# Kernel optimization log

Hardware: AMD Instinct MI355X
Metric: run time of the kernel (lower is better)

## Reference

```python
import jax, jax.numpy as jnp
import numpy as np

EMBED_DIM = 64
D_STATE = 16
D_CONV = 4
EXPAND = 2
DT_RANK = 8
D_INNER = EXPAND * EMBED_DIM  # 128
B_, T_, H_, W_ = 4, 16, 16, 16


def _causal_dwconv(x, w, b):
    # x: (B, D, L), w: (D, 1, K) depthwise causal conv (left pad K-1), matches
    # torch conv1d(padding=K-1)[..., :L]
    K = w.shape[-1]
    y = jax.lax.conv_general_dilated(
        x, w, window_strides=(1,), padding=[(K - 1, 0)],
        feature_group_count=x.shape[1], dimension_numbers=('NCH', 'OIH', 'NCH'))
    return y + b[None, :, None]


def _selective_scan(u, delta, A, Bm, Cm, D):
    # u, delta: (B, d, L); A: (d, n); Bm, Cm: (B, n, L); D: (d,)
    dA = jnp.exp(jnp.einsum('bdl,dn->lbdn', delta, A))      # (L,B,d,n)
    dBu = jnp.einsum('bdl,bnl,bdl->lbdn', delta, Bm, u)     # (L,B,d,n)
    h0 = jnp.zeros(dA.shape[1:], dA.dtype)

    def step(h, xs):
        dA_t, dBu_t = xs
        h = dA_t * h + dBu_t
        return h, h

    _, hs = jax.lax.scan(step, h0, (dA, dBu))               # (L,B,d,n)
    y = jnp.einsum('lbdn,bnl->bdl', hs, Cm)
    return y + u * D[None, :, None]


def _mamba_branch(x, z, conv_w, conv_b, xproj_w, dtproj_w, dtproj_b, A_log, D):
    # x, z: (B, d_inner, L)
    x = jax.nn.silu(_causal_dwconv(x, conv_w, conv_b))
    x_dbl = jnp.einsum('bdl,ed->bel', x, xproj_w)           # e = dt_rank + 2*n
    dt = x_dbl[:, :DT_RANK]
    Bm = x_dbl[:, DT_RANK:DT_RANK + D_STATE]
    Cm = x_dbl[:, DT_RANK + D_STATE:]
    delta = jax.nn.softplus(jnp.einsum('brl,dr->bdl', dt, dtproj_w) + dtproj_b[None, :, None])
    A = -jnp.exp(A_log)
    y = _selective_scan(x, delta, A, Bm, Cm, D)
    return y * jax.nn.silu(z)


def _conv3d(x, w, b, pad):
    y = jax.lax.conv_general_dilated(
        x, w, window_strides=(1, 1, 1), padding=[(pad, pad)] * 3,
        dimension_numbers=('NCDHW', 'OIDHW', 'NCDHW'))
    return y + b[None, :, None, None, None]


def setup_inputs() -> dict:
    key = jax.random.key(0)
    ks = jax.random.split(key, 24)
    s = 0.02
    d, n, r, K, C = D_INNER, D_STATE, DT_RANK, D_CONV, EMBED_DIM
    inp = {
        'x': jax.random.normal(ks[0], (B_, C, T_, H_, W_), jnp.float32),
        'in_proj_w': jax.random.normal(ks[1], (2 * d, C), jnp.float32) * s,
        'conv_w': jax.random.normal(ks[2], (d, 1, K), jnp.float32) * s,
        'conv_b': jnp.zeros((d,), jnp.float32),
        'xproj_w': jax.random.normal(ks[3], (r + 2 * n, d), jnp.float32) * s,
        'dtproj_w': jax.random.normal(ks[4], (d, r), jnp.float32) * s,
        'dtproj_b': jax.random.normal(ks[5], (d,), jnp.float32) * s,
        'A_log': jnp.tile(jnp.log(jnp.arange(1, n + 1, dtype=jnp.float32))[None, :], (d, 1)),
        'D': jnp.ones((d,), jnp.float32),
        'conv_w_b': jax.random.normal(ks[6], (d, 1, K), jnp.float32) * s,
        'conv_b_b': jnp.zeros((d,), jnp.float32),
        'xproj_w_b': jax.random.normal(ks[7], (r + 2 * n, d), jnp.float32) * s,
        'dtproj_w_b': jax.random.normal(ks[8], (d, r), jnp.float32) * s,
        'dtproj_b_b': jax.random.normal(ks[9], (d,), jnp.float32) * s,
        'A_b_log': jnp.tile(jnp.log(jnp.arange(1, n + 1, dtype=jnp.float32))[None, :], (d, 1)),
        'D_b': jnp.ones((d,), jnp.float32),
        'out_proj_w': jax.random.normal(ks[10], (C, d), jnp.float32) * s,
        'proj_w': jax.random.normal(ks[11], (C, C, 3, 3, 3), jnp.float32) * s,
        'proj_b': jnp.zeros((C,), jnp.float32),
        'norm_w': jax.random.normal(ks[12], (C, C, 1, 1, 1), jnp.float32) * s,
        'norm_b': jnp.zeros((C,), jnp.float32),
    }
    return inp


def reference(x, in_proj_w, conv_w, conv_b, xproj_w, dtproj_w, dtproj_b, A_log, D,
              conv_w_b, conv_b_b, xproj_w_b, dtproj_w_b, dtproj_b_b, A_b_log, D_b,
              out_proj_w, proj_w, proj_b, norm_w, norm_b):
    residual = x
    B, C, T, H, W = x.shape
    # SpectralPriority scan: b c t h w -> b c (h w t)
    seq = x.transpose(0, 1, 3, 4, 2).reshape(B, C, H * W * T)
    # bimamba v2
    xz = jnp.einsum('bcl,ec->bel', seq, in_proj_w)          # (B, 2*d_inner, L)
    x_f, z_f = xz[:, :D_INNER], xz[:, D_INNER:]
    y_f = _mamba_branch(x_f, z_f, conv_w, conv_b, xproj_w, dtproj_w, dtproj_b, A_log, D)
    xz_r = jnp.flip(xz, -1)
    x_b, z_b = xz_r[:, :D_INNER], xz_r[:, D_INNER:]
    y_b = _mamba_branch(x_b, z_b, conv_w_b, conv_b_b, xproj_w_b, dtproj_w_b, dtproj_b_b, A_b_log, D_b)
    out = y_f + jnp.flip(y_b, -1)                           # (B, d_inner, L)
    out = jnp.einsum('bdl,cd->blc', out, out_proj_w)        # (B, L, C)
    x_recon = out.reshape(B, C, T, H, W)
    x3 = _conv3d(x_recon, proj_w, proj_b, pad=1)
    return _conv3d(x3 + residual, norm_w, norm_b, pad=0)
```

## Files before the change

### kernel.cpp

```cpp
#include <hip/hip_runtime.h>


#define NL 4096

typedef unsigned short u16;
typedef unsigned int u32;
typedef __attribute__((ext_vector_type(8))) short bf16x8;
typedef __attribute__((ext_vector_type(4))) float f32x4;

__device__ __forceinline__ float siluf_(float x) {
  return x * __builtin_amdgcn_rcpf(1.f + __expf(-x));
}
__device__ __forceinline__ float softplusf_(float x) {
  return (x > 20.f) ? x : __logf(1.f + __expf(x));
}
__device__ __forceinline__ u16 f2bf(float f) {
  u32 u = __float_as_uint(f);
  u += 0x7fffu + ((u >> 16) & 1u);
  return (u16)(u >> 16);
}
__device__ __forceinline__ float bflo(u32 v) { return __uint_as_float(v << 16); }
__device__ __forceinline__ float bfhi(u32 v) { return __uint_as_float(v & 0xFFFF0000u); }

__device__ __forceinline__ float rowsum16_(float p) {
  int q;
  q = __builtin_amdgcn_mov_dpp(__float_as_int(p), 0x121, 0xf, 0xf, false);
  p += __int_as_float(q);
  q = __builtin_amdgcn_mov_dpp(__float_as_int(p), 0x122, 0xf, 0xf, false);
  p += __int_as_float(q);
  q = __builtin_amdgcn_mov_dpp(__float_as_int(p), 0x124, 0xf, 0xf, false);
  p += __int_as_float(q);
  q = __builtin_amdgcn_mov_dpp(__float_as_int(p), 0x128, 0xf, 0xf, false);
  p += __int_as_float(q);
  return p;
}

#define OXZ  0u
#define OUCF 1048576u
#define OUCB 1572864u
#define ODLF 2424832u
#define ODLB 2949120u
#define OYF  3473408u
#define OYB  3997696u
#define OO   4521984u
#define OO2  5046272u
#define OX4  5308416u
#define PER_B 5570560u

#define NCH 64
#define CL  64

__global__ __launch_bounds__(256) void kxz(
    const float* __restrict__ x, const float* __restrict__ wip,
    float* __restrict__ ws, int b0) {
  int bi = blockIdx.y, gb = b0 + bi;
  float* s = ws + (size_t)bi * PER_B;
  int bid = blockIdx.x;
  int h = bid >> 4, w = bid & 15;
  int tid = threadIdx.x;
  __shared__ float xs[64][16];
  for (int i = tid; i < 1024; i += 256) {
    int c = i >> 4, t = i & 15;
    xs[c][t] = x[(size_t)(gb * 64 + c) * NL + t * 256 + h * 16 + w];
  }
  __syncthreads();
  int e = tid;
  float acc[16];
#pragma unroll
  for (int t = 0; t < 16; ++t) acc[t] = 0.f;
  for (int c = 0; c < 64; ++c) {
    float wv = wip[e * 64 + c];
#pragma unroll
    for (int t = 0; t < 16; ++t) acc[t] = fmaf(wv, xs[c][t], acc[t]);
  }
  float4* dst = (float4*)(s + OXZ + (size_t)e * NL + h * 256 + w * 16);
#pragma unroll
  for (int q = 0; q < 4; ++q)
    dst[q] = make_float4(acc[q * 4], acc[q * 4 + 1], acc[q * 4 + 2], acc[q * 4 + 3]);
}

__global__ __launch_bounds__(256) void k2prep(
    const float* __restrict__ cwf, const float* __restrict__ cbf,
    const float* __restrict__ xpf, const float* __restrict__ dtwf,
    const float* __restrict__ dtbf,
    const float* __restrict__ cwb, const float* __restrict__ cbb,
    const float* __restrict__ xpb, const float* __restrict__ dtwb,
    const float* __restrict__ dtbb,
    float* __restrict__ ws) {
  int bi = blockIdx.y;
  float* s = ws + (size_t)bi * PER_B;
  int bx = blockIdx.x;
  int lt = bx >> 1, dir = bx & 1;
  int l0 = lt * 32;
  int lout0 = dir ? (127 - lt) * 32 : l0;
  int tid = threadIdx.x;

  __shared__ float pool[128 * 40];
  __shared__ u16 uct[32][136];
  float (*X)[40] = (float(*)[40])pool;

  for (int i = tid; i < 128 * 38; i += 256) {
    int d = i / 38, j = i - d * 38;
    int l = l0 - 3 + j;
    X[d][j] = (l >= 0 && l < NL) ? s[OXZ + (size_t)d * NL + l] : 0.f;
  }
  __syncthreads();

  const float* cw = dir ? cwb : cwf;
  const float* cb = dir ? cbb : cbf;
  u16* ucg = (u16*)(s + (dir ? OUCB : OUCF));
  for (int i = tid; i < 128 * 32; i += 256) {
    int d = i >> 5, li = i & 31;
    float a = cb[d];
    if (dir == 0) {
#pragma unroll
      for (int k = 0; k < 4; ++k) a = fmaf(cw[d * 4 + k], X[d][li + k], a);
    } else {
#pragma unroll
      for (int k = 0; k < 4; ++k) a = fmaf(cw[d * 4 + k], X[d][37 - li - k], a);
    }
    a = siluf_(a);
    u16 ab = f2bf(a);
    uct[li][d] = ab;
    ucg[(size_t)d * NL + lout0 + li] = ab;
  }
  __syncthreads();

  float* xds = pool;
  {
    int wid = tid >> 6, lane = tid & 63;
    int n16 = lane & 15, kg = lane >> 4;
    const float* xp = dir ? xpb : xpf;
#pragma unroll
    for (int rep = 0; rep < 2; ++rep) {
      int id = wid + rep * 4;
      if (id < 6) {
        int et = id >> 1, lt2 = id & 1;
        f32x4 acc = {};
#pragma unroll
        for (int ks = 0; ks < 4; ++ks) {
          bf16x8 bfrag = *(const bf16x8*)&uct[lt2 * 16 + n16][ks * 32 + kg * 8];
          int e = et * 16 + n16;
          int ec = (e < 40) ? e : 39;
          const float* pa = xp + ec * 128 + ks * 32 + kg * 8;
          float4 a0 = *(const float4*)pa;
          float4 a1 = *(const float4*)(pa + 4);
          bf16x8 af;
          af[0] = (short)f2bf(a0.x); af[1] = (short)f2bf(a0.y);
          af[2] = (short)f2bf(a0.z); af[3] = (short)f2bf(a0.w);
          af[4] = (short)f2bf(a1.x); af[5] = (short)f2bf(a1.y);
          af[6] = (short)f2bf(a1.z); af[7] = (short)f2bf(a1.w);
          acc = __builtin_amdgcn_mfma_f32_16x16x32_bf16(af, bfrag, acc, 0, 0, 0);
        }
#pragma unroll
        for (int rg = 0; rg < 4; ++rg) {
          int e = et * 16 + kg * 4 + rg;
          if (e < 40) xds[e * 33 + lt2 * 16 + n16] = acc[rg];
        }
      }
    }
  }
  __syncthreads();

  const float* dtw = dir ? dtwb : dtwf;
  const float* dtb = dir ? dtbb : dtbf;
  u16* dlg = (u16*)(s + (dir ? ODLB : ODLF));
  for (int i = tid; i < 128 * 32; i += 256) {
    int d = i >> 5, li = i & 31;
    float pre = dtb[d];
#pragma unroll
    for (int r = 0; r < 8; ++r)
      pre = fmaf(dtw[d * 8 + r], xds[r * 33 + li], pre);
    dlg[(size_t)d * NL + lout0 + li] = f2bf(softplusf_(pre));
  }
  u16* bctp = (u16*)(s + OO2);
  for (int i = tid; i < 32 * 32; i += 256) {
    int li = i >> 5, k = i & 31;
    bctp[((size_t)dir * 4096 + lout0 + li) * 32 + k] = f2bf(xds[(8 + k) * 33 + li]);
  }
}

__global__ __launch_bounds__(256) void kscanA(
    const float* __restrict__ Alf, const float* __restrict__ Alb,
    float* __restrict__ ws) {
  int bi = blockIdx.y;
  float* s = ws + (size_t)bi * PER_B;
  int xid = blockIdx.x;
  int chunk = xid >> 4, dir = (xid >> 3) & 1, d8 = xid & 7;
  int tid = threadIdx.x;
  int wv = tid >> 6, lane = tid & 63;
  int n = lane & 15, g = lane >> 4;
  int d = d8 * 16 + wv * 4 + g;
  int l0 = chunk * CL;
  __shared__ float bl[CL * 32];
  {
    const u16* bctp = (const u16*)(s + OO2) + ((size_t)dir * 4096 + l0) * 32;
    for (int i = tid; i < CL * 32; i += 256)
      bl[i] = __uint_as_float(((u32)bctp[i]) << 16);
  }
  __syncthreads();
  const u16* ucp = (const u16*)(s + (dir ? OUCB : OUCF)) + (size_t)d * NL + l0;
  const u16* dlp = (const u16*)(s + (dir ? ODLB : ODLF)) + (size_t)d * NL + l0;
  float A = -__expf((dir ? Alb : Alf)[d * 16 + n]);
  float P = 1.f, S = 0.f;
  for (int i0 = 0; i0 < CL; i0 += 8) {
    uint4 dq = *(const uint4*)(dlp + i0);
    uint4 uq = *(const uint4*)(ucp + i0);
    float dv[8] = {bflo(dq.x), bfhi(dq.x), bflo(dq.y), bfhi(dq.y),
                   bflo(dq.z), bfhi(dq.z), bflo(dq.w), bfhi(dq.w)};
    float uv[8] = {bflo(uq.x), bfhi(uq.x), bflo(uq.y), bfhi(uq.y),
                   bflo(uq.z), bfhi(uq.z), bflo(uq.w), bfhi(uq.w)};
#pragma unroll
    for (int j = 0; j < 8; ++j) {
      float dA = __expf(dv[j] * A);
      S = fmaf(dA, S, dv[j] * bl[(i0 + j) * 32 + n] * uv[j]);
      P *= dA;
    }
  }
  size_t cidx = ((size_t)(chunk * 2 + dir) * 128 + d) * 16 + n;
  s[OO + cidx] = P;
  s[OO + 262144u + cidx] = S;
}

__global__ __launch_bounds__(64) void kscanB(float* __restrict__ ws) {
  int bi = blockIdx.y;
  float* s = ws + (size_t)bi * PER_B;
  int dir = blockIdx.x >> 5, dblk = blockIdx.x & 31;
  int tid = threadIdx.x;
  size_t base = (size_t)dir * 2048 + dblk * 64 + tid;
  float carry = 0.f;
#pragma unroll 4
  for (int c = 0; c < NCH; ++c) {
    size_t idx = (size_t)c * 4096 + base;
    float pv = s[OO + idx], sv = s[OO + 262144u + idx];
    s[OO + 262144u + idx] = carry;
    carry = fmaf(pv, carry, sv);
  }
}

__global__ __launch_bounds__(256) void kscanC(
    const float* __restrict__ Alf, const float* __restrict__ Df,
    const float* __restrict__ Alb, const float* __restrict__ Db,
    float* __restrict__ ws) {
  int bi = blockIdx.y;
  float* s = ws + (size_t)bi * PER_B;
  int xid = blockIdx.x;
  int chunk = xid >> 4, dir = (xid >> 3) & 1, d8 = xid & 7;
  int tid = threadIdx.x;
  int wv = tid >> 6, lane = tid & 63;
  int n = lane & 15, g = lane >> 4;
  int d = d8 * 16 + wv * 4 + g;
  int l0 = chunk * CL;
  __shared__ float bl[CL * 32];
  __shared__ float ps[16][65];
  {
    const u16* bctp = (const u16*)(s + OO2) + ((size_t)dir * 4096 + l0) * 32;
    for (int i = tid; i < CL * 32; i += 256)
      bl[i] = __uint_as_float(((u32)bctp[i]) << 16);
  }
  __syncthreads();
  const u16* ucp = (const u16*)(s + (dir ? OUCB : OUCF)) + (size_t)d * NL + l0;
  const u16* dlp = (const u16*)(s + (dir ? ODLB : ODLF)) + (size_t)d * NL + l0;
  float* ybase = s + (dir ? OYB : OYF);
  float A = -__expf((dir ? Alb : Alf)[d * 16 + n]);
  float Dv = (dir ? Db : Df)[d];
  size_t cidx = ((size_t)(chunk * 2 + dir) * 128 + d) * 16 + n;
  float h = s[OO + 262144u + cidx];
  int prow = wv * 4 + g;
  for (int i0 = 0; i0 < CL; i0 += 8) {
    uint4 dq = *(const uint4*)(dlp + i0);
    uint4 uq = *(const uint4*)(ucp + i0);
    float dv[8] = {bflo(dq.x), bfhi(dq.x), bflo(dq.y), bfhi(dq.y),
                   bflo(dq.z), bfhi(dq.z), bflo(dq.w), bfhi(dq.w)};
    float uv[8] = {bflo(uq.x), bfhi(uq.x), bflo(uq.y), bfhi(uq.y),
                   bflo(uq.z), bfhi(uq.z), bflo(uq.w), bfhi(uq.w)};
#pragma unroll
    for (int j = 0; j < 8; ++j) {
      int i = i0 + j;
      float dA = __expf(dv[j] * A);
      h = fmaf(dA, h, dv[j] * bl[i * 32 + n] * uv[j]);
      float p = rowsum16_(h * bl[i * 32 + 16 + n]);
      if (n == 0) ps[prow][i] = fmaf(uv[j], Dv, p);
    }
  }
  __syncthreads();
  for (int i = tid; i < 16 * CL; i += 256) {
    int row = i >> 6, col = i & 63;
    ybase[(size_t)(d8 * 16 + row) * NL + l0 + col] = ps[row][col];
  }
}

__global__ __launch_bounds__(256) void koutg(
    const float* __restrict__ wout, float* __restrict__ ws) {
  int bi = blockIdx.y;
  float* s = ws + (size_t)bi * PER_B;
  int lt = blockIdx.x;
  int l0 = lt * 32;
  int tid = threadIdx.x;
  __shared__ float ot[128][32];
  __shared__ float ot2[64][33];
  for (int i = tid; i < 128 * 32; i += 256) {
    int d = i >> 5, li = i & 31;
    int l = l0 + li;
    float z = s[OXZ + (size_t)(128 + d) * NL + l];
    float v = s[OYF + (size_t)d * NL + l] + s[OYB + (size_t)d * NL + (NL - 1 - l)];
    ot[d][li] = v * siluf_(z);
  }
  __syncthreads();
  {
    int li = tid & 31, cg = tid >> 5;
    float acc[8];
#pragma unroll
    for (int j = 0; j < 8; ++j) acc[j] = 0.f;
    for (int d4 = 0; d4 < 128; d4 += 4) {
      float o0 = ot[d4][li], o1 = ot[d4 + 1][li];
      float o2v = ot[d4 + 2][li], o3 = ot[d4 + 3][li];
#pragma unroll
      for (int j = 0; j < 8; ++j) {
        float4 w4 = *(const float4*)&wout[(cg * 8 + j) * 128 + d4];
        acc[j] = fmaf(w4.x, o0, fmaf(w4.y, o1, fmaf(w4.z, o2v, fmaf(w4.w, o3, acc[j]))));
      }
    }
#pragma unroll
    for (int j = 0; j < 8; ++j) ot2[cg * 8 + j][li] = acc[j];
  }
  __syncthreads();
  for (int i = tid; i < 32 * 64; i += 256) {
    int li = i >> 6, c = i & 63;
    s[OO2 + (size_t)(l0 + li) * 64 + c] = ot2[c][li];
  }
}

__global__ __launch_bounds__(256) void kprepw(
    const float* __restrict__ pw, float* __restrict__ ws) {
  int off = blockIdx.x;
  u16* wb = (u16*)(ws + OO);
  int tid = threadIdx.x;
  for (int i = tid; i < 4096; i += 256) {
    int co = i >> 6, ci = i & 63;
    wb[off * 4096 + i] = f2bf(pw[(size_t)(co * 64 + ci) * 27 + off]);
  }
}

__global__ __launch_bounds__(256) void kconv3(
    const float* __restrict__ pb, const float* __restrict__ xin,
    float* __restrict__ ws, int b0) {
  int bi = blockIdx.y, gb = b0 + bi;
  float* s = ws + (size_t)bi * PER_B;
  int t = blockIdx.x >> 2, hq = blockIdx.x & 3;
  int h0 = hq * 4;
  int tid = threadIdx.x;
  const u16* wb = (const u16*)(ws + OO);
  const float* xr = s + OO2;

  __shared__ u16 Xs[3 * 6 * 18 * 72];
  {
    u32* xz32 = (u32*)Xs;
    for (int i = tid; i < 3 * 6 * 18 * 72 / 2; i += 256) xz32[i] = 0u;
  }
  __syncthreads();
  {
    int ci = tid >> 2, wq = tid & 3;
    for (int row = 0; row < 18; ++row) {
      int tt = row / 6, hh = row - tt * 6;
      int ts = t + tt - 1, hs = h0 + hh - 1;
      if (ts < 0 || ts > 15 || hs < 0 || hs > 15) continue;
      float4 v = *(const float4*)(xr + (size_t)ci * NL + ts * 256 + hs * 16 + wq * 4);
      int rb = (tt * 6 + hh) * 18 + 1 + wq * 4;
      Xs[(rb + 0) * 72 + ci] = f2bf(v.x);
      Xs[(rb + 1) * 72 + ci] = f2bf(v.y);
      Xs[(rb + 2) * 72 + ci] = f2bf(v.z);
      Xs[(rb + 3) * 72 + ci] = f2bf(v.w);
    }
  }
  __syncthreads();

  int wid = tid >> 6, lane = tid & 63;
  int cb = wid >> 1, lb = wid & 1;
  int n16 = lane & 15, kg = lane >> 4;
  f32x4 acc[2][2] = {};

  const u16* wbA = wb + (size_t)(cb * 32 + n16) * 64 + kg * 8;
  for (int kt = 0; kt < 3; ++kt)
    for (int kh = 0; kh < 3; ++kh) {
      int rbase = (kt * 6 + lb * 2 + kh) * 18 + n16;
#pragma unroll
      for (int kw = 0; kw < 3; ++kw) {
        int off = (kt * 3 + kh) * 3 + kw;
        int r0 = rbase + kw;
        const u16* pa = wbA + off * 4096;
#pragma unroll
        for (int st = 0; st < 2; ++st) {
          int kb = st * 32;
          bf16x8 a0 = *(const bf16x8*)(pa + kb);
          bf16x8 a1 = *(const bf16x8*)(pa + 16 * 64 + kb);
          bf16x8 b0 = *(const bf16x8*)(&Xs[r0 * 72 + kb + kg * 8]);
          bf16x8 b1 = *(const bf16x8*)(&Xs[(r0 + 18) * 72 + kb + kg * 8]);
          acc[0][0] = __builtin_amdgcn_mfma_f32_16x16x32_bf16(a0, b0, acc[0][0], 0, 0, 0);
          acc[0][1] = __builtin_amdgcn_mfma_f32_16x16x32_bf16(a0, b1, acc[0][1], 0, 0, 0);
          acc[1][0] = __builtin_amdgcn_mfma_f32_16x16x32_bf16(a1, b0, acc[1][0], 0, 0, 0);
          acc[1][1] = __builtin_amdgcn_mfma_f32_16x16x32_bf16(a1, b1, acc[1][1], 0, 0, 0);
        }
      }
    }

#pragma unroll
  for (int c2 = 0; c2 < 2; ++c2) {
#pragma unroll
    for (int l2 = 0; l2 < 2; ++l2) {
      int lg = t * 256 + (h0 + lb * 2 + l2) * 16 + n16;
#pragma unroll
      for (int rg = 0; rg < 4; ++rg) {
        int co = cb * 32 + c2 * 16 + kg * 4 + rg;
        float v = acc[c2][l2][rg] + pb[co] +
                  xin[(size_t)(gb * 64 + co) * NL + lg];
        s[OX4 + (size_t)co * NL + lg] = v;
      }
    }
  }
}

__global__ __launch_bounds__(256) void knorm(
    const float* __restrict__ nw, const float* __restrict__ nb,
    float* __restrict__ out, float* __restrict__ ws, int b0) {
  int bi = blockIdx.y, gb = b0 + bi;
  float* s = ws + (size_t)bi * PER_B;
  int pt = blockIdx.x;
  int p0 = pt * 64;
  int tid = threadIdx.x;
  __shared__ float xs[64][64];
  for (int i = tid; i < 4096; i += 256) {
    int ci = i >> 6, p = i & 63;
    xs[ci][p] = s[OX4 + (size_t)ci * NL + p0 + p];
  }
  __syncthreads();
  int co = tid >> 2, pq = tid & 3;
  float acc[16];
#pragma unroll
  for (int j = 0; j < 16; ++j) acc[j] = 0.f;
  for (int ci = 0; ci < 64; ci += 4) {
    float4 w4 = *(const float4*)&nw[co * 64 + ci];
    float wv[4] = {w4.x, w4.y, w4.z, w4.w};
#pragma unroll
    for (int cc = 0; cc < 4; ++cc) {
      const float4* row = (const float4*)&xs[ci + cc][pq * 16];
      float4 a = row[0], b = row[1], c = row[2], e = row[3];
      acc[0] = fmaf(wv[cc], a.x, acc[0]);  acc[1] = fmaf(wv[cc], a.y, acc[1]);
      acc[2] = fmaf(wv[cc], a.z, acc[2]);  acc[3] = fmaf(wv[cc], a.w, acc[3]);
      acc[4] = fmaf(wv[cc], b.x, acc[4]);  acc[5] = fmaf(wv[cc], b.y, acc[5]);
      acc[6] = fmaf(wv[cc], b.z, acc[6]);  acc[7] = fmaf(wv[cc], b.w, acc[7]);
      acc[8] = fmaf(wv[cc], c.x, acc[8]);  acc[9] = fmaf(wv[cc], c.y, acc[9]);
      acc[10] = fmaf(wv[cc], c.z, acc[10]); acc[11] = fmaf(wv[cc], c.w, acc[11]);
      acc[12] = fmaf(wv[cc], e.x, acc[12]); acc[13] = fmaf(wv[cc], e.y, acc[13]);
      acc[14] = fmaf(wv[cc], e.z, acc[14]); acc[15] = fmaf(wv[cc], e.w, acc[15]);
    }
  }
  float bias = nb[co];
  float4* dst = (float4*)(out + (size_t)(gb * 64 + co) * NL + p0 + pq * 16);
#pragma unroll
  for (int q = 0; q < 4; ++q)
    dst[q] = make_float4(acc[q * 4] + bias, acc[q * 4 + 1] + bias,
                         acc[q * 4 + 2] + bias, acc[q * 4 + 3] + bias);
}

extern "C" void kernel_launch(void* const* d_in, const int* in_sizes, int n_in,
                              void* d_out, int out_size, void* d_ws, size_t ws_size,
                              hipStream_t stream) {
  const float* x    = (const float*)d_in[0];
  const float* wip  = (const float*)d_in[1];
  const float* cwf  = (const float*)d_in[2];
  const float* cbf  = (const float*)d_in[3];
  const float* xpf  = (const float*)d_in[4];
  const float* dtwf = (const float*)d_in[5];
  const float* dtbf = (const float*)d_in[6];
  const float* Alf  = (const float*)d_in[7];
  const float* Df   = (const float*)d_in[8];
  const float* cwb  = (const float*)d_in[9];
  const float* cbb  = (const float*)d_in[10];
  const float* xpb  = (const float*)d_in[11];
  const float* dtwb = (const float*)d_in[12];
  const float* dtbb = (const float*)d_in[13];
  const float* Alb  = (const float*)d_in[14];
  const float* Db   = (const float*)d_in[15];
  const float* wout = (const float*)d_in[16];
  const float* pw   = (const float*)d_in[17];
  const float* pb   = (const float*)d_in[18];
  const float* nw   = (const float*)d_in[19];
  const float* nb   = (const float*)d_in[20];

  const size_t PER_B_BYTES = (size_t)PER_B * 4;
  int bcnt;
  if (ws_size >= 4 * PER_B_BYTES) bcnt = 4;
  else if (ws_size >= PER_B_BYTES) bcnt = 1;
  else return;
  int passes = 4 / bcnt;

  float* ws = (float*)d_ws;
  for (int p = 0; p < passes; ++p) {
    int b0 = p * bcnt;
    kxz   <<<dim3(256, bcnt), 256, 0, stream>>>(x, wip, ws, b0);
    k2prep<<<dim3(256, bcnt), 256, 0, stream>>>(cwf, cbf, xpf, dtwf, dtbf,
                                                cwb, cbb, xpb, dtwb, dtbb, ws);
    kscanA<<<dim3(1024, bcnt), 256, 0, stream>>>(Alf, Alb, ws);
    kscanB<<<dim3(64, bcnt), 64, 0, stream>>>(ws);
    kscanC<<<dim3(1024, bcnt), 256, 0, stream>>>(Alf, Df, Alb, Db, ws);
    koutg <<<dim3(128, bcnt), 256, 0, stream>>>(wout, ws);
    kprepw<<<dim3(27), 256, 0, stream>>>(pw, ws);
    kconv3<<<dim3(64, bcnt), 256, 0, stream>>>(pb, x, ws, b0);
    knorm <<<dim3(64, bcnt), 256, 0, stream>>>(nw, nb, (float*)d_out, ws, b0);
  }
}
```

Baseline: 267.8 us.

## Fuse 1x1 norm conv into conv3 epilogue and use MFMA for out_proj

The pointwise norm convolution now runs inside the 3x3x3 conv kernel. The residual-added conv output is staged in shared memory, so the separate knorm kernel and its global round trip through OX4 are gone. The out-projection in koutg is rewritten to use bf16 MFMA instructions instead of scalar FMAs, and kprepw is hoisted out of the batch loop into a separate workspace region. This cuts kernel launches and global traffic. In exchange, out_proj now uses bf16 precision and the conv3 blocks carry an extra epilogue phase.

```diff
diff --git a/kernel.cpp b/kernel.cpp
--- a/kernel.cpp
+++ b/kernel.cpp
@@ -44,7 +44,6 @@
 #define OYB  3997696u
 #define OO   4521984u
 #define OO2  5046272u
-#define OX4  5308416u
 #define PER_B 5570560u
 
 #define NCH 64
@@ -297,44 +296,45 @@
   int lt = blockIdx.x;
   int l0 = lt * 32;
   int tid = threadIdx.x;
-  __shared__ float ot[128][32];
-  __shared__ float ot2[64][33];
+  __shared__ u16 otb[32][136];
   for (int i = tid; i < 128 * 32; i += 256) {
     int d = i >> 5, li = i & 31;
     int l = l0 + li;
     float z = s[OXZ + (size_t)(128 + d) * NL + l];
     float v = s[OYF + (size_t)d * NL + l] + s[OYB + (size_t)d * NL + (NL - 1 - l)];
-    ot[d][li] = v * siluf_(z);
-  }
-  __syncthreads();
-  {
-    int li = tid & 31, cg = tid >> 5;
-    float acc[8];
-#pragma unroll
-    for (int j = 0; j < 8; ++j) acc[j] = 0.f;
-    for (int d4 = 0; d4 < 128; d4 += 4) {
-      float o0 = ot[d4][li], o1 = ot[d4 + 1][li];
-      float o2v = ot[d4 + 2][li], o3 = ot[d4 + 3][li];
-#pragma unroll
-      for (int j = 0; j < 8; ++j) {
-        float4 w4 = *(const float4*)&wout[(cg * 8 + j) * 128 + d4];
-        acc[j] = fmaf(w4.x, o0, fmaf(w4.y, o1, fmaf(w4.z, o2v, fmaf(w4.w, o3, acc[j]))));
-      }
-    }
-#pragma unroll
-    for (int j = 0; j < 8; ++j) ot2[cg * 8 + j][li] = acc[j];
-  }
-  __syncthreads();
-  for (int i = tid; i < 32 * 64; i += 256) {
-    int li = i >> 6, c = i & 63;
-    s[OO2 + (size_t)(l0 + li) * 64 + c] = ot2[c][li];
+    otb[li][d] = f2bf(v * siluf_(z));
+  }
+  __syncthreads();
+  int wid = tid >> 6, lane = tid & 63;
+  int n16 = lane & 15, kg = lane >> 4;
+  f32x4 acc[2] = {};
+  const float* wr = wout + (size_t)(wid * 16 + n16) * 128 + kg * 8;
+#pragma unroll
+  for (int ks = 0; ks < 4; ++ks) {
+    const float* pa = wr + ks * 32;
+    float4 a0 = *(const float4*)pa;
+    float4 a1 = *(const float4*)(pa + 4);
+    bf16x8 af;
+    af[0] = (short)f2bf(a0.x); af[1] = (short)f2bf(a0.y);
+    af[2] = (short)f2bf(a0.z); af[3] = (short)f2bf(a0.w);
+    af[4] = (short)f2bf(a1.x); af[5] = (short)f2bf(a1.y);
+    af[6] = (short)f2bf(a1.z); af[7] = (short)f2bf(a1.w);
+    bf16x8 b0 = *(const bf16x8*)&otb[n16][ks * 32 + kg * 8];
+    bf16x8 b1 = *(const bf16x8*)&otb[16 + n16][ks * 32 + kg * 8];
+    acc[0] = __builtin_amdgcn_mfma_f32_16x16x32_bf16(af, b0, acc[0], 0, 0, 0);
+    acc[1] = __builtin_amdgcn_mfma_f32_16x16x32_bf16(af, b1, acc[1], 0, 0, 0);
+  }
+#pragma unroll
+  for (int l2 = 0; l2 < 2; ++l2) {
+    float4 st = make_float4(acc[l2][0], acc[l2][1], acc[l2][2], acc[l2][3]);
+    *(float4*)&s[OO2 + (size_t)(l0 + l2 * 16 + n16) * 64 + wid * 16 + kg * 4] = st;
   }
 }
 
 __global__ __launch_bounds__(256) void kprepw(
-    const float* __restrict__ pw, float* __restrict__ ws) {
+    const float* __restrict__ pw, float* __restrict__ wdst) {
   int off = blockIdx.x;
-  u16* wb = (u16*)(ws + OO);
+  u16* wb = (u16*)wdst;
   int tid = threadIdx.x;
   for (int i = tid; i < 4096; i += 256) {
     int co = i >> 6, ci = i & 63;
@@ -343,17 +343,19 @@
 }
 
 __global__ __launch_bounds__(256) void kconv3(
-    const float* __restrict__ pb, const float* __restrict__ xin,
+    const float* __restrict__ pb, const float* __restrict__ nw,
+    const float* __restrict__ nb, const float* __restrict__ xin,
+    float* __restrict__ out, const u16* __restrict__ wb,
     float* __restrict__ ws, int b0) {
   int bi = blockIdx.y, gb = b0 + bi;
   float* s = ws + (size_t)bi * PER_B;
   int t = blockIdx.x >> 2, hq = blockIdx.x & 3;
   int h0 = hq * 4;
   int tid = threadIdx.x;
-  const u16* wb = (const u16*)(ws + OO);
   const float* xr = s + OO2;
 
   __shared__ u16 Xs[3 * 6 * 18 * 72];
+  float* cx = (float*)Xs;
   {
     u32* xz32 = (u32*)Xs;
     for (int i = tid; i < 3 * 6 * 18 * 72 / 2; i += 256) xz32[i] = 0u;
@@ -403,64 +405,57 @@
         }
       }
     }
+  __syncthreads();
 
 #pragma unroll
   for (int c2 = 0; c2 < 2; ++c2) {
 #pragma unroll
     for (int l2 = 0; l2 < 2; ++l2) {
-      int lg = t * 256 + (h0 + lb * 2 + l2) * 16 + n16;
+      int lp = (lb * 2 + l2) * 16 + n16;
+      int lg = t * 256 + h0 * 16 + lp;
 #pragma unroll
       for (int rg = 0; rg < 4; ++rg) {
         int co = cb * 32 + c2 * 16 + kg * 4 + rg;
-        float v = acc[c2][l2][rg] + pb[co] +
-                  xin[(size_t)(gb * 64 + co) * NL + lg];
-        s[OX4 + (size_t)co * NL + lg] = v;
+        cx[co * 65 + lp] = acc[c2][l2][rg] + pb[co] +
+                           xin[(size_t)(gb * 64 + co) * NL + lg];
       }
     }
   }
-}
-
-__global__ __launch_bounds__(256) void knorm(
-    const float* __restrict__ nw, const float* __restrict__ nb,
-    float* __restrict__ out, float* __restrict__ ws, int b0) {
-  int bi = blockIdx.y, gb = b0 + bi;
-  float* s = ws + (size_t)bi * PER_B;
-  int pt = blockIdx.x;
-  int p0 = pt * 64;
-  int tid = threadIdx.x;
-  __shared__ float xs[64][64];
-  for (int i = tid; i < 4096; i += 256) {
-    int ci = i >> 6, p = i & 63;
-    xs[ci][p] = s[OX4 + (size_t)ci * NL + p0 + p];
-  }
-  __syncthreads();
-  int co = tid >> 2, pq = tid & 3;
-  float acc[16];
-#pragma unroll
-  for (int j = 0; j < 16; ++j) acc[j] = 0.f;
-  for (int ci = 0; ci < 64; ci += 4) {
-    float4 w4 = *(const float4*)&nw[co * 64 + ci];
-    float wv[4] = {w4.x, w4.y, w4.z, w4.w};
-#pragma unroll
-    for (int cc = 0; cc < 4; ++cc) {
-      const float4* row = (const float4*)&xs[ci + cc][pq * 16];
-      float4 a = row[0], b = row[1], c = row[2], e = row[3];
-      acc[0] = fmaf(wv[cc], a.x, acc[0]);  acc[1] = fmaf(wv[cc], a.y, acc[1]);
-      acc[2] = fmaf(wv[cc], a.z, acc[2]);  acc[3] = fmaf(wv[cc], a.w, acc[3]);
-      acc[4] = fmaf(wv[cc], b.x, acc[4]);  acc[5] = fmaf(wv[cc], b.y, acc[5]);
-      acc[6] = fmaf(wv[cc], b.z, acc[6]);  acc[7] = fmaf(wv[cc], b.w, acc[7]);
-      acc[8] = fmaf(wv[cc], c.x, acc[8]);  acc[9] = fmaf(wv[cc], c.y, acc[9]);
-      acc[10] = fmaf(wv[cc], c.z, acc[10]); acc[11] = fmaf(wv[cc], c.w, acc[11]);
-      acc[12] = fmaf(wv[cc], e.x, acc[12]); acc[13] = fmaf(wv[cc], e.y, acc[13]);
-      acc[14] = fmaf(wv[cc], e.z, acc[14]); acc[15] = fmaf(wv[cc], e.w, acc[15]);
-    }
-  }
-  float bias = nb[co];
-  float4* dst = (float4*)(out + (size_t)(gb * 64 + co) * NL + p0 + pq * 16);
-#pragma unroll
-  for (int q = 0; q < 4; ++q)
-    dst[q] = make_float4(acc[q * 4] + bias, acc[q * 4 + 1] + bias,
-                         acc[q * 4 + 2] + bias, acc[q * 4 + 3] + bias);
+  __syncthreads();
+
+  {
+    int co2 = tid >> 2, pq = tid & 3;
+    float mac[16];
+#pragma unroll
+    for (int j = 0; j < 16; ++j) mac[j] = 0.f;
+    for (int ci = 0; ci < 64; ci += 4) {
+      float4 w4 = *(const float4*)&nw[co2 * 64 + ci];
+      float wv[4] = {w4.x, w4.y, w4.z, w4.w};
+#pragma unroll
+      for (int cc = 0; cc < 4; ++cc) {
+        const float* row = &cx[(ci + cc) * 65 + pq * 16];
+        float4 a = *(const float4*)&row[0];
+        float4 b = *(const float4*)&row[4];
+        float4 c = *(const float4*)&row[8];
+        float4 e = *(const float4*)&row[12];
+        mac[0] = fmaf(wv[cc], a.x, mac[0]);   mac[1] = fmaf(wv[cc], a.y, mac[1]);
+        mac[2] = fmaf(wv[cc], a.z, mac[2]);   mac[3] = fmaf(wv[cc], a.w, mac[3]);
+        mac[4] = fmaf(wv[cc], b.x, mac[4]);   mac[5] = fmaf(wv[cc], b.y, mac[5]);
+        mac[6] = fmaf(wv[cc], b.z, mac[6]);   mac[7] = fmaf(wv[cc], b.w, mac[7]);
+        mac[8] = fmaf(wv[cc], c.x, mac[8]);   mac[9] = fmaf(wv[cc], c.y, mac[9]);
+        mac[10] = fmaf(wv[cc], c.z, mac[10]); mac[11] = fmaf(wv[cc], c.w, mac[11]);
+        mac[12] = fmaf(wv[cc], e.x, mac[12]); mac[13] = fmaf(wv[cc], e.y, mac[13]);
+        mac[14] = fmaf(wv[cc], e.z, mac[14]); mac[15] = fmaf(wv[cc], e.w, mac[15]);
+      }
+    }
+    float bias = nb[co2];
+    float4* dst = (float4*)(out + (size_t)(gb * 64 + co2) * NL +
+                            t * 256 + h0 * 16 + pq * 16);
+#pragma unroll
+    for (int q = 0; q < 4; ++q)
+      dst[q] = make_float4(mac[q * 4] + bias, mac[q * 4 + 1] + bias,
+                           mac[q * 4 + 2] + bias, mac[q * 4 + 3] + bias);
+  }
 }
 
 extern "C" void kernel_launch(void* const* d_in, const int* in_sizes, int n_in,
@@ -489,13 +484,16 @@
   const float* nb   = (const float*)d_in[20];
 
   const size_t PER_B_BYTES = (size_t)PER_B * 4;
+  const size_t WB_BYTES = 27u * 64u * 64u * 2u;
   int bcnt;
-  if (ws_size >= 4 * PER_B_BYTES) bcnt = 4;
-  else if (ws_size >= PER_B_BYTES) bcnt = 1;
+  if (ws_size >= 4 * PER_B_BYTES + WB_BYTES) bcnt = 4;
+  else if (ws_size >= PER_B_BYTES + WB_BYTES) bcnt = 1;
   else return;
   int passes = 4 / bcnt;
 
   float* ws = (float*)d_ws;
+  float* wsW = ws + (size_t)bcnt * PER_B;
+  kprepw<<<dim3(27), 256, 0, stream>>>(pw, wsW);
   for (int p = 0; p < passes; ++p) {
     int b0 = p * bcnt;
     kxz   <<<dim3(256, bcnt), 256, 0, stream>>>(x, wip, ws, b0);
@@ -505,8 +503,7 @@
     kscanB<<<dim3(64, bcnt), 64, 0, stream>>>(ws);
     kscanC<<<dim3(1024, bcnt), 256, 0, stream>>>(Alf, Df, Alb, Db, ws);
     koutg <<<dim3(128, bcnt), 256, 0, stream>>>(wout, ws);
-    kprepw<<<dim3(27), 256, 0, stream>>>(pw, ws);
-    kconv3<<<dim3(64, bcnt), 256, 0, stream>>>(pb, x, ws, b0);
-    knorm <<<dim3(64, bcnt), 256, 0, stream>>>(nw, nb, (float*)d_out, ws, b0);
-  }
-}
+    kconv3<<<dim3(64, bcnt), 256, 0, stream>>>(pb, nw, nb, x, (float*)d_out,
+                                               (const u16*)wsW, ws, b0);
+  }
+}
```

Measured after the change: 265.0 us. About the same (-1.0%).
